# Kernel tuning notes

Measured on AMD Instinct MI355X. Metric: run time of the kernel, lower is better.

## Reference

```python
import jax, jax.numpy as jnp
import numpy as np

N_EXPERTS = 8
TOP_K = 2
D_MODEL = 1024
D_FF = 4 * D_MODEL

def setup_inputs() -> dict:
    key = jax.random.key(0)
    ks = jax.random.split(key, 5)
    s_in = 1.0 / np.sqrt(D_MODEL)
    s_ff = 1.0 / np.sqrt(D_FF)
    return {
        "x": jax.random.normal(ks[0], (2, 2048, D_MODEL), dtype=jnp.float32),
        "Wr": jax.random.normal(ks[1], (N_EXPERTS, D_MODEL), dtype=jnp.float32) * s_in,
        "W1": jax.random.normal(ks[2], (N_EXPERTS, D_FF, D_MODEL), dtype=jnp.float32) * s_in,
        "W2": jax.random.normal(ks[3], (N_EXPERTS, D_MODEL, D_FF), dtype=jnp.float32) * s_ff,
        "W3": jax.random.normal(ks[4], (N_EXPERTS, D_FF, D_MODEL), dtype=jnp.float32) * s_in,
    }

def reference(x, Wr, W1, W2, W3):
    B, S, D = x.shape
    T = B * S
    xf = x.reshape(T, D)
    logits = xf @ Wr.T                         # [T, E]
    probs = jax.nn.softmax(logits, axis=-1)
    top_p, top_i = jax.lax.top_k(probs, TOP_K)  # [T, K]
    top_p = top_p / jnp.sum(top_p, axis=-1, keepdims=True)
    # per-token combine weight for each expert: [T, E]
    onehot = jax.nn.one_hot(top_i, N_EXPERTS, dtype=x.dtype)  # [T, K, E]
    cw = jnp.einsum('tke,tk->te', onehot, top_p)
    out = jnp.zeros_like(xf)
    for e in range(N_EXPERTS):  # fixed small structural loop over experts
        h = jax.nn.silu(xf @ W1[e].T) * (xf @ W3[e].T)  # [T, F]
        y = h @ W2[e].T                                 # [T, D]
        out = out + cw[:, e:e+1] * y
    importance = jnp.sum(probs, axis=0)                 # [E]
    load = jnp.sum(jnp.sum(onehot, axis=1), axis=0)     # [E]
    aux_loss = jnp.sum(importance * load) * (N_EXPERTS / (T ** 2 + 1e-06))
    return out.reshape(B, S, D), aux_loss
```

## Files before the change

kernel.cpp:

```cpp
#include <hip/hip_runtime.h>

#define T_TOK 4096
#define DM 1024
#define DF 4096
#define NE 8
#define BM 256
#define RCAP 10240
#define MAXT 40
#define MAXT2 80
#define ACH_B 32768
#define CHUNK_B 8192

typedef _Float16 f16x8 __attribute__((ext_vector_type(8)));
typedef float f32x4 __attribute__((ext_vector_type(4)));

#define MFMA16(a, b, c) __builtin_amdgcn_mfma_f32_16x16x32_f16(a, b, c, 0, 0, 0)
#define RAW_BAR() __builtin_amdgcn_s_barrier()
#define VMCNT(n) asm volatile("s_waitcnt vmcnt(" #n ")" ::: "memory")

__device__ __forceinline__ ushort f2h_bits(float f) {
    _Float16 h = (_Float16)f;
    return __builtin_bit_cast(unsigned short, h);
}

__device__ __forceinline__ unsigned int pk2(float a, float b) {
    return __builtin_bit_cast(unsigned int, __builtin_amdgcn_cvt_pkrtz(a, b));
}

__device__ __forceinline__ uint4 pack8f(float4 a, float4 b) {
    uint4 r;
    r.x = pk2(a.x, a.y); r.y = pk2(a.z, a.w);
    r.z = pk2(b.x, b.y); r.w = pk2(b.z, b.w);
    return r;
}

__device__ __forceinline__ void gll16(const void* g, void* l) {
    __builtin_amdgcn_global_load_lds(
        (const __attribute__((address_space(1))) unsigned int*)g,
        (__attribute__((address_space(3))) unsigned int*)l, 16, 0, 0);
}

__global__ __launch_bounds__(256) void k_init(float* __restrict__ out,
                                              int* __restrict__ misc,
                                              int* __restrict__ row_tok) {
    int i = blockIdx.x * 256 + threadIdx.x;
    if (i < T_TOK * DM + 1) out[i] = 0.f;
    if (i < RCAP) row_tok[i] = -1;
    if (i < 256) misc[i] = 0;
}

__global__ __launch_bounds__(64) void k_router(const float* __restrict__ x,
                                               const float* __restrict__ Wr,
                                               float* __restrict__ probs,
                                               int* __restrict__ topi,
                                               float* __restrict__ topw,
                                               int* __restrict__ cnt) {
    int t = blockIdx.x;
    int lane = threadIdx.x;
    const float* xr = x + (size_t)t * DM;
    float s[NE];
#pragma unroll
    for (int e = 0; e < NE; e++) s[e] = 0.f;
    for (int j = lane; j < DM; j += 64) {
        float xv = xr[j];
#pragma unroll
        for (int e = 0; e < NE; e++) s[e] += xv * Wr[e * DM + j];
    }
#pragma unroll
    for (int off = 32; off > 0; off >>= 1) {
#pragma unroll
        for (int e = 0; e < NE; e++) s[e] += __shfl_xor(s[e], off, 64);
    }
    if (lane == 0) {
        float mx = s[0];
#pragma unroll
        for (int e = 1; e < NE; e++) mx = fmaxf(mx, s[e]);
        float ex[NE], sum = 0.f;
#pragma unroll
        for (int e = 0; e < NE; e++) { ex[e] = expf(s[e] - mx); sum += ex[e]; }
        float inv = 1.f / sum;
        float p[NE];
#pragma unroll
        for (int e = 0; e < NE; e++) { p[e] = ex[e] * inv; probs[t * NE + e] = p[e]; }
        int i0 = 0;
#pragma unroll
        for (int e = 1; e < NE; e++) if (p[e] > p[i0]) i0 = e;
        int i1 = (i0 == 0) ? 1 : 0;
#pragma unroll
        for (int e = 0; e < NE; e++) if (e != i0 && p[e] > p[i1]) i1 = e;
        float w0 = p[i0], w1 = p[i1], winv = 1.f / (w0 + w1);
        topi[2 * t] = i0;     topw[2 * t] = w0 * winv;
        topi[2 * t + 1] = i1; topw[2 * t + 1] = w1 * winv;
        atomicAdd(&cnt[i0], 1);
        atomicAdd(&cnt[i1], 1);
    }
}

__global__ __launch_bounds__(256) void k_scan(const float* __restrict__ probs,
                                              const int* __restrict__ cnt,
                                              int* __restrict__ poff,
                                              int* __restrict__ texp,
                                              int* __restrict__ texp2,
                                              int* __restrict__ ntp,
                                              float* __restrict__ aux_out) {
    __shared__ float red[256 * NE];
    int tid = threadIdx.x;
    float part[NE];
#pragma unroll
    for (int e = 0; e < NE; e++) part[e] = 0.f;
    for (int t = tid; t < T_TOK; t += 256) {
#pragma unroll
        for (int e = 0; e < NE; e++) part[e] += probs[t * NE + e];
    }
#pragma unroll
    for (int e = 0; e < NE; e++) red[tid * NE + e] = part[e];
    __syncthreads();
    for (int s2 = 128; s2 > 0; s2 >>= 1) {
        if (tid < s2) {
#pragma unroll
            for (int e = 0; e < NE; e++) red[tid * NE + e] += red[(tid + s2) * NE + e];
        }
        __syncthreads();
    }
    if (tid == 0) {
        float al = 0.f;
#pragma unroll
        for (int e = 0; e < NE; e++) al += red[e] * (float)cnt[e];
        *aux_out = al * (8.0f / (16777216.0f + 1e-6f));
        int run = 0, tix = 0;
        for (int e = 0; e < NE; e++) {
            poff[e] = run;
            int nt = (cnt[e] + BM - 1) / BM;
            for (int i = 0; i < nt; i++) texp[tix++] = e;
            run += nt * BM;
        }
        ntp[0] = run / BM;
        ntp[1] = run / 128;
        for (int j = 0; j < MAXT2; j++) texp2[j] = (j >> 1) < tix ? texp[j >> 1] : 0;
    }
}

__global__ __launch_bounds__(256) void k_assign(const int* __restrict__ topi,
                                                const float* __restrict__ topw,
                                                const int* __restrict__ poff,
                                                int* __restrict__ fill,
                                                int* __restrict__ row_tok,
                                                float* __restrict__ row_w) {
    int t = blockIdx.x * 256 + threadIdx.x;
    if (t >= T_TOK) return;
#pragma unroll
    for (int k = 0; k < 2; k++) {
        int e = topi[2 * t + k];
        int pos = atomicAdd(&fill[e], 1);
        int r = poff[e] + pos;
        row_tok[r] = t;
        row_w[r] = topw[2 * t + k];
    }
}

__global__ __launch_bounds__(256) void k_convert(const float* __restrict__ src,
                                                 ushort* __restrict__ dst,
                                                 int row_len) {
    int nk = row_len >> 6;
    int kt = blockIdx.x, rt = blockIdx.y;
    int tid = threadIdx.x;
    int r = tid >> 2, c0 = (tid & 3) * 16;
    const float* s = src + (size_t)(rt * 64 + r) * row_len + kt * 64 + c0;
    float4 v0 = *(const float4*)(s);
    float4 v1 = *(const float4*)(s + 4);
    float4 v2 = *(const float4*)(s + 8);
    float4 v3 = *(const float4*)(s + 12);
    char* chunk = (char*)dst + ((size_t)rt * nk + kt) * CHUNK_B;
    int sw = (r & 7) << 4;
    *(uint4*)(chunk + r * 128 + ((2 * c0) ^ sw)) = pack8f(v0, v1);
    *(uint4*)(chunk + r * 128 + ((2 * c0 + 16) ^ sw)) = pack8f(v2, v3);
}

__global__ __launch_bounds__(512) void k_gather_t(const float* __restrict__ x,
                                                  const int* __restrict__ row_tok,
                                                  ushort* __restrict__ xg) {
    int kt = blockIdx.x, rt = blockIdx.y;
    int tid = threadIdx.x;
    int r = tid >> 1, c0 = (tid & 1) * 32;
    int tok = row_tok[rt * BM + r];
    char* chunk = (char*)xg + ((size_t)rt * 16 + kt) * ACH_B;
    int sw = (r & 7) << 4;
    if (tok >= 0) {
        const float* s = x + (size_t)tok * DM + kt * 64 + c0;
#pragma unroll
        for (int j = 0; j < 4; j++) {
            float4 va = *(const float4*)(s + j * 8);
            float4 vb = *(const float4*)(s + j * 8 + 4);
            *(uint4*)(chunk + r * 128 + ((c0 * 2 + j * 16) ^ sw)) = pack8f(va, vb);
        }
    } else {
        uint4 z = {0, 0, 0, 0};
#pragma unroll
        for (int j = 0; j < 4; j++)
            *(uint4*)(chunk + r * 128 + ((c0 * 2 + j * 16) ^ sw)) = z;
    }
}

__global__ __launch_bounds__(512, 2) void k_g1(const ushort* __restrict__ xg,
                                               const ushort* __restrict__ W1h,
                                               const ushort* __restrict__ W3h,
                                               const int* __restrict__ texp,
                                               const int* __restrict__ ntp,
                                               ushort* __restrict__ hbuf) {
    __shared__ __align__(16) char lds[131072];
    int b = blockIdx.x;
    int sz = (b & 7) * 160 + (b >> 3);
    int ct = sz / MAXT, rt = sz % MAXT;
    if (rt >= ntp[0]) return;
    int e = texp[rt];
    int tid = threadIdx.x, lane = tid & 63, wv = tid >> 6;
    int wr = wv >> 1, wc = wv & 1;

    const char* Ac  = (const char*)xg + (size_t)rt * 16 * ACH_B;
    const char* B1c = (const char*)W1h + ((size_t)(e * 64 + ct * 2) * 16) * CHUNK_B;
    const char* B3c = (const char*)W3h + ((size_t)(e * 64 + ct * 2) * 16) * CHUNK_B;

    const f32x4 fz = {0.f, 0.f, 0.f, 0.f};
    f32x4 acc1[4][4], acc3[4][4];
#pragma unroll
    for (int m = 0; m < 4; m++)
#pragma unroll
        for (int n = 0; n < 4; n++) { acc1[m][n] = fz; acc3[m][n] = fz; }

    f16x8 af[4], bf[4];
    int kb_base = (lane >> 4) * 16;

#define ST_A(kt_, b_, h_) {                                                        \
        const char* s_ = Ac + (kt_) * ACH_B + (h_) * 16384 + wv * 2048 + lane * 16; \
        char* d_ = lds + (b_) * 65536 + (h_) * 16384 + wv * 2048;                   \
        gll16(s_, d_); gll16(s_ + 1024, d_ + 1024); }
#define ST_B(Bc_, kt_, b_, off_) {                                                          \
        gll16(Bc_ + (kt_) * 8192 + wv * 1024 + lane * 16,                                    \
              lds + (b_) * 65536 + (off_) + wv * 1024);                                      \
        gll16(Bc_ + 131072 + (kt_) * 8192 + wv * 1024 + lane * 16,                           \
              lds + (b_) * 65536 + (off_) + 8192 + wv * 1024); }
#define DS_A(b_, ks_) _Pragma("unroll") for (int m = 0; m < 4; m++) {              \
        int r_ = wr * 64 + m * 16 + (lane & 15);                                   \
        af[m] = *(const f16x8*)(lds + (b_) * 65536 + r_ * 128 +                    \
                                 (((ks_) * 64 + kb_base) ^ ((r_ & 7) << 4))); }
#define DS_B(b_, off_, ks_) _Pragma("unroll") for (int n = 0; n < 4; n++) {        \
        int c_ = wc * 64 + n * 16 + (lane & 15);                                   \
        bf[n] = *(const f16x8*)(lds + (b_) * 65536 + (off_) + c_ * 128 +           \
                                 (((ks_) * 64 + kb_base) ^ ((c_ & 7) << 4))); }
#define MM(accX) _Pragma("unroll") for (int n = 0; n < 4; n++)                     \
        _Pragma("unroll") for (int m = 0; m < 4; m++)                              \
            accX[m][n] = MFMA16(af[m], bf[n], accX[m][n]);

    ST_A(0, 0, 0); ST_A(0, 0, 1); ST_B(B1c, 0, 0, 32768); ST_B(B3c, 0, 0, 49152);
    VMCNT(2);
    RAW_BAR();

    for (int it = 0; it < 8; ++it) {
        int t1 = 2 * it + 1;
        int t2 = 2 * it + 2;
        DS_A(0, 0); DS_B(0, 32768, 0);
        ST_A(t1, 1, 0);
        RAW_BAR();
        __builtin_amdgcn_s_setprio(1); MM(acc1); __builtin_amdgcn_s_setprio(0);
        VMCNT(2);
        RAW_BAR();
        DS_B(0, 49152, 0);
        ST_A(t1, 1, 1);
        RAW_BAR();
        __builtin_amdgcn_s_setprio(1); MM(acc3); __builtin_amdgcn_s_setprio(0);
        RAW_BAR();
        DS_A(0, 1); DS_B(0, 32768, 1);
        ST_B(B1c, t1, 1, 32768);
        RAW_BAR();
        __builtin_amdgcn_s_setprio(1); MM(acc1); __builtin_amdgcn_s_setprio(0);
        RAW_BAR();
        DS_B(0, 49152, 1);
        ST_B(B3c, t1, 1, 49152);
        RAW_BAR();
        __builtin_amdgcn_s_setprio(1); MM(acc3); __builtin_amdgcn_s_setprio(0);
        VMCNT(2);
        RAW_BAR();
        DS_A(1, 0); DS_B(1, 32768, 0);
        if (it < 7) ST_A(t2, 0, 0);
        RAW_BAR();
        __builtin_amdgcn_s_setprio(1); MM(acc1); __builtin_amdgcn_s_setprio(0);
        if (it < 7) { VMCNT(2); } else { VMCNT(0); }
        RAW_BAR();
        DS_B(1, 49152, 0);
        if (it < 7) ST_A(t2, 0, 1);
        RAW_BAR();
        __builtin_amdgcn_s_setprio(1); MM(acc3); __builtin_amdgcn_s_setprio(0);
        RAW_BAR();
        DS_A(1, 1); DS_B(1, 32768, 1);
        if (it < 7) ST_B(B1c, t2, 0, 32768);
        RAW_BAR();
        __builtin_amdgcn_s_setprio(1); MM(acc1); __builtin_amdgcn_s_setprio(0);
        RAW_BAR();
        DS_B(1, 49152, 1);
        if (it < 7) ST_B(B3c, t2, 0, 49152);
        RAW_BAR();
        __builtin_amdgcn_s_setprio(1); MM(acc3); __builtin_amdgcn_s_setprio(0);
        if (it < 7) { VMCNT(2); }
        RAW_BAR();
    }
#undef ST_A
#undef ST_B
#undef DS_A
#undef DS_B
#undef MM

#pragma unroll
    for (int m = 0; m < 4; m++) {
#pragma unroll
        for (int i = 0; i < 4; i++) {
            int rl = wr * 64 + m * 16 + (lane >> 4) * 4 + i;
            int sw = (rl & 7) << 4;
#pragma unroll
            for (int n = 0; n < 4; n++) {
                int fl = wc * 64 + n * 16 + (lane & 15);
                float a1 = acc1[m][n][i], a3 = acc3[m][n][i];
                float h = (a1 / (1.f + expf(-a1))) * a3;
                char* hc = (char*)hbuf + ((size_t)rt * 64 + ct * 2 + (fl >> 6)) * ACH_B;
                *(ushort*)(hc + rl * 128 + ((2 * (fl & 63)) ^ sw)) = f2h_bits(h);
            }
        }
    }
}

__global__ __launch_bounds__(256, 2) void k_g2(const ushort* __restrict__ hbuf,
                                               const ushort* __restrict__ W2h,
                                               const int* __restrict__ texp2,
                                               const int* __restrict__ ntp,
                                               const int* __restrict__ row_tok,
                                               const float* __restrict__ row_w,
                                               float* __restrict__ out) {
    __shared__ __align__(16) char lds[73728];
    int b = blockIdx.x;
    int sz = (b & 7) * 160 + (b >> 3);
    int ct = sz / MAXT2, rt2 = sz % MAXT2;
    if (rt2 >= ntp[1]) return;
    int e = texp2[rt2];
    int tid = threadIdx.x, lane = tid & 63, wv = tid >> 6;
    int wr = wv >> 1, wc = wv & 1;

    const char* Ac = (const char*)hbuf + ((size_t)(rt2 >> 1) * 64) * ACH_B + (rt2 & 1) * 16384;
    const char* Bc = (const char*)W2h + ((size_t)(e * 16 + ct) * 64) * CHUNK_B;

    const f32x4 fz = {0.f, 0.f, 0.f, 0.f};
    f32x4 acc[4][2];
#pragma unroll
    for (int m = 0; m < 4; m++)
#pragma unroll
        for (int n = 0; n < 2; n++) acc[m][n] = fz;

    f16x8 af[4], bf[2];
    int kb_base = (lane >> 4) * 16;

#define BUF3(t_) (((t_) % 3) * 24576)
#define ST2_A(kt_) {                                                                 \
        const char* s_ = Ac + (size_t)(kt_) * ACH_B + wv * 4096 + lane * 16;         \
        char* d_ = lds + BUF3(kt_) + wv * 4096;                                      \
        gll16(s_, d_); gll16(s_ + 1024, d_ + 1024);                                  \
        gll16(s_ + 2048, d_ + 2048); gll16(s_ + 3072, d_ + 3072); }
#define ST2_B(kt_) {                                                                 \
        const char* s_ = Bc + (size_t)(kt_) * 8192 + wv * 2048 + lane * 16;          \
        char* d_ = lds + BUF3(kt_) + 16384 + wv * 2048;                              \
        gll16(s_, d_); gll16(s_ + 1024, d_ + 1024); }
#define DS2_A(bo_, ks_) _Pragma("unroll") for (int m = 0; m < 4; m++) {              \
        int r_ = wr * 64 + m * 16 + (lane & 15);                                     \
        af[m] = *(const f16x8*)(lds + (bo_) + r_ * 128 +                             \
                                 (((ks_) * 64 + kb_base) ^ ((r_ & 7) << 4))); }
#define DS2_B(bo_, ks_) _Pragma("unroll") for (int n = 0; n < 2; n++) {              \
        int c_ = wc * 32 + n * 16 + (lane & 15);                                     \
        bf[n] = *(const f16x8*)(lds + (bo_) + 16384 + c_ * 128 +                     \
                                 (((ks_) * 64 + kb_base) ^ ((c_ & 7) << 4))); }
#define MM2() _Pragma("unroll") for (int n = 0; n < 2; n++)                          \
        _Pragma("unroll") for (int m = 0; m < 4; m++)                                \
            acc[m][n] = MFMA16(af[m], bf[n], acc[m][n]);

    ST2_A(0); ST2_B(0);
    ST2_A(1); ST2_B(1);
    VMCNT(6);
    RAW_BAR();

    for (int t = 0; t < 64; ++t) {
        int bo = BUF3(t);
        DS2_A(bo, 0); DS2_B(bo, 0);
        if (t < 62) ST2_A(t + 2);
        RAW_BAR();
        __builtin_amdgcn_s_setprio(1); MM2(); __builtin_amdgcn_s_setprio(0);
        RAW_BAR();
        DS2_A(bo, 1); DS2_B(bo, 1);
        if (t < 62) ST2_B(t + 2);
        RAW_BAR();
        __builtin_amdgcn_s_setprio(1); MM2(); __builtin_amdgcn_s_setprio(0);
        if (t < 62) { VMCNT(6); }
        else if (t == 62) { VMCNT(0); }
        RAW_BAR();
    }
#undef BUF3
#undef ST2_A
#undef ST2_B
#undef DS2_A
#undef DS2_B
#undef MM2

#pragma unroll
    for (int m = 0; m < 4; m++) {
#pragma unroll
        for (int i = 0; i < 4; i++) {
            int rr = rt2 * 128 + wr * 64 + m * 16 + (lane >> 4) * 4 + i;
            int tok = row_tok[rr];
            if (tok >= 0) {
                float w = row_w[rr];
                float* orow = out + (size_t)tok * DM + ct * 64 + wc * 32 + (lane & 15);
#pragma unroll
                for (int n = 0; n < 2; n++) atomicAdd(&orow[n * 16], w * acc[m][n][i]);
            }
        }
    }
}

extern "C" void kernel_launch(void* const* d_in, const int* in_sizes, int n_in,
                              void* d_out, int out_size, void* d_ws, size_t ws_size,
                              hipStream_t stream) {
    (void)in_sizes; (void)n_in; (void)out_size; (void)ws_size;
    const float* x  = (const float*)d_in[0];
    const float* Wr = (const float*)d_in[1];
    const float* W1 = (const float*)d_in[2];
    const float* W2 = (const float*)d_in[3];
    const float* W3 = (const float*)d_in[4];
    float* out = (float*)d_out;
    char* ws = (char*)d_ws;

    int* misc  = (int*)ws;
    int* cnt   = misc;
    int* fill  = misc + 8;
    int* poff  = misc + 16;
    int* texp  = misc + 24;
    int* texp2 = misc + 64;
    int* ntp   = misc + 144;
    int*    topi    = (int*)(ws + 1024);
    float*  topw    = (float*)(ws + 33792);
    float*  probs   = (float*)(ws + 66560);
    int*    row_tok = (int*)(ws + 197632);
    float*  row_w   = (float*)(ws + 238592);
    ushort* hbuf    = (ushort*)(ws + 279552);
    ushort* W1h     = (ushort*)(ws + 84165632);
    ushort* W3h     = (ushort*)(ws + 151274496);
    ushort* xg      = (ushort*)(ws + 218383360);
    ushort* W2h     = (ushort*)(ws + 218383360);

    k_init<<<(T_TOK * DM + 1 + 255) / 256, 256, 0, stream>>>(out, misc, row_tok);
    k_router<<<T_TOK, 64, 0, stream>>>(x, Wr, probs, topi, topw, cnt);
    k_scan<<<1, 256, 0, stream>>>(probs, cnt, poff, texp, texp2, ntp, out + (size_t)T_TOK * DM);
    k_assign<<<(T_TOK + 255) / 256, 256, 0, stream>>>(topi, topw, poff, fill, row_tok, row_w);

    k_convert<<<dim3(16, 512), 256, 0, stream>>>(W1, W1h, DM);
    k_convert<<<dim3(16, 512), 256, 0, stream>>>(W3, W3h, DM);
    k_gather_t<<<dim3(16, MAXT), 512, 0, stream>>>(x, row_tok, xg);
    k_g1<<<32 * MAXT, 512, 0, stream>>>(xg, W1h, W3h, texp, ntp, hbuf);
    k_convert<<<dim3(64, 128), 256, 0, stream>>>(W2, W2h, DF);
    k_g2<<<8 * MAXT2 * 2, 256, 0, stream>>>(hbuf, W2h, texp2, ntp, row_tok, row_w, out);
}
```

Before: 677.9 us.

## Map GEMM blocks to XCDs by expert via precomputed block tables

The scan kernel now builds block-to-tile tables for both grouped GEMMs. Each table routes all tiles of one expert to the same blockIdx residue mod 8, and so to the same XCD, spilling to the next XCD once 160 slots fill. The aim is to keep each expert's weights in a single XCD's L2 and so cut duplicate weight fetches. The cost is a serial single-thread loop in k_scan and an extra indirect load per block, and load across XCDs may be uneven when experts get unequal token counts.

Measured after the change: 820.4 us. 1.21x slower.

```diff
diff --git a/kernel.cpp b/kernel.cpp
--- a/kernel.cpp
+++ b/kernel.cpp
@@ -101,7 +101,8 @@
                                               int* __restrict__ poff,
                                               int* __restrict__ texp,
                                               int* __restrict__ texp2,
-                                              int* __restrict__ ntp,
+                                              int* __restrict__ bmap1,
+                                              int* __restrict__ bmap2,
                                               float* __restrict__ aux_out) {
     __shared__ float red[256 * NE];
     int tid = threadIdx.x;
@@ -122,21 +123,46 @@
         }
         __syncthreads();
     }
+    for (int s = tid; s < 1280; s += 256) { bmap1[s] = -1; bmap2[s] = -1; }
+    __syncthreads();
     if (tid == 0) {
         float al = 0.f;
 #pragma unroll
         for (int e = 0; e < NE; e++) al += red[e] * (float)cnt[e];
         *aux_out = al * (8.0f / (16777216.0f + 1e-6f));
         int run = 0, tix = 0;
+        int tstart[NE], ntv[NE];
         for (int e = 0; e < NE; e++) {
             poff[e] = run;
             int nt = (cnt[e] + BM - 1) / BM;
+            tstart[e] = tix; ntv[e] = nt;
             for (int i = 0; i < nt; i++) texp[tix++] = e;
             run += nt * BM;
         }
-        ntp[0] = run / BM;
-        ntp[1] = run / 128;
         for (int j = 0; j < MAXT2; j++) texp2[j] = (j >> 1) < tix ? texp[j >> 1] : 0;
+        int u1[NE] = {0, 0, 0, 0, 0, 0, 0, 0};
+        for (int e = 0; e < NE; e++)
+            for (int i = 0; i < ntv[e]; i++) {
+                int rt = tstart[e] + i;
+                for (int ct = 0; ct < 32; ct++) {
+                    int k = e, tr = 0;
+                    while (u1[k] >= 160 && tr < 8) { k = (k + 1) & 7; tr++; }
+                    bmap1[k + 8 * u1[k]] = (rt << 5) | ct;
+                    u1[k]++;
+                }
+            }
+        int u2[NE] = {0, 0, 0, 0, 0, 0, 0, 0};
+        for (int e = 0; e < NE; e++)
+            for (int i = 0; i < ntv[e]; i++)
+                for (int h = 0; h < 2; h++) {
+                    int rt2 = (tstart[e] + i) * 2 + h;
+                    for (int ct = 0; ct < 16; ct++) {
+                        int k = e, tr = 0;
+                        while (u2[k] >= 160 && tr < 8) { k = (k + 1) & 7; tr++; }
+                        bmap2[k + 8 * u2[k]] = (rt2 << 4) | ct;
+                        u2[k]++;
+                    }
+                }
     }
 }
 
@@ -205,13 +231,12 @@
                                                const ushort* __restrict__ W1h,
                                                const ushort* __restrict__ W3h,
                                                const int* __restrict__ texp,
-                                               const int* __restrict__ ntp,
+                                               const int* __restrict__ bmap1,
                                                ushort* __restrict__ hbuf) {
     __shared__ __align__(16) char lds[131072];
-    int b = blockIdx.x;
-    int sz = (b & 7) * 160 + (b >> 3);
-    int ct = sz / MAXT, rt = sz % MAXT;
-    if (rt >= ntp[0]) return;
+    int mcode = bmap1[blockIdx.x];
+    if (mcode < 0) return;
+    int rt = mcode >> 5, ct = mcode & 31;
     int e = texp[rt];
     int tid = threadIdx.x, lane = tid & 63, wv = tid >> 6;
     int wr = wv >> 1, wc = wv & 1;
@@ -330,15 +355,14 @@
 __global__ __launch_bounds__(256, 2) void k_g2(const ushort* __restrict__ hbuf,
                                                const ushort* __restrict__ W2h,
                                                const int* __restrict__ texp2,
-                                               const int* __restrict__ ntp,
+                                               const int* __restrict__ bmap2,
                                                const int* __restrict__ row_tok,
                                                const float* __restrict__ row_w,
                                                float* __restrict__ out) {
     __shared__ __align__(16) char lds[73728];
-    int b = blockIdx.x;
-    int sz = (b & 7) * 160 + (b >> 3);
-    int ct = sz / MAXT2, rt2 = sz % MAXT2;
-    if (rt2 >= ntp[1]) return;
+    int mcode = bmap2[blockIdx.x];
+    if (mcode < 0) return;
+    int rt2 = mcode >> 4, ct = mcode & 15;
     int e = texp2[rt2];
     int tid = threadIdx.x, lane = tid & 63, wv = tid >> 6;
     int wr = wv >> 1, wc = wv & 1;
@@ -439,27 +463,29 @@
     int* poff  = misc + 16;
     int* texp  = misc + 24;
     int* texp2 = misc + 64;
-    int* ntp   = misc + 144;
     int*    topi    = (int*)(ws + 1024);
     float*  topw    = (float*)(ws + 33792);
     float*  probs   = (float*)(ws + 66560);
     int*    row_tok = (int*)(ws + 197632);
     float*  row_w   = (float*)(ws + 238592);
-    ushort* hbuf    = (ushort*)(ws + 279552);
-    ushort* W1h     = (ushort*)(ws + 84165632);
-    ushort* W3h     = (ushort*)(ws + 151274496);
-    ushort* xg      = (ushort*)(ws + 218383360);
-    ushort* W2h     = (ushort*)(ws + 218383360);
+    int*    bmap1   = (int*)(ws + 279552);
+    int*    bmap2   = (int*)(ws + 284672);
+    ushort* hbuf    = (ushort*)(ws + 294912);
+    ushort* W1h     = (ushort*)(ws + 84180992);
+    ushort* W3h     = (ushort*)(ws + 151289856);
+    ushort* xg      = (ushort*)(ws + 218398720);
+    ushort* W2h     = (ushort*)(ws + 218398720);
 
     k_init<<<(T_TOK * DM + 1 + 255) / 256, 256, 0, stream>>>(out, misc, row_tok);
     k_router<<<T_TOK, 64, 0, stream>>>(x, Wr, probs, topi, topw, cnt);
-    k_scan<<<1, 256, 0, stream>>>(probs, cnt, poff, texp, texp2, ntp, out + (size_t)T_TOK * DM);
+    k_scan<<<1, 256, 0, stream>>>(probs, cnt, poff, texp, texp2, bmap1, bmap2,
+                                  out + (size_t)T_TOK * DM);
     k_assign<<<(T_TOK + 255) / 256, 256, 0, stream>>>(topi, topw, poff, fill, row_tok, row_w);
 
     k_convert<<<dim3(16, 512), 256, 0, stream>>>(W1, W1h, DM);
     k_convert<<<dim3(16, 512), 256, 0, stream>>>(W3, W3h, DM);
     k_gather_t<<<dim3(16, MAXT), 512, 0, stream>>>(x, row_tok, xg);
-    k_g1<<<32 * MAXT, 512, 0, stream>>>(xg, W1h, W3h, texp, ntp, hbuf);
+    k_g1<<<1280, 512, 0, stream>>>(xg, W1h, W3h, texp, bmap1, hbuf);
     k_convert<<<dim3(64, 128), 256, 0, stream>>>(W2, W2h, DF);
-    k_g2<<<8 * MAXT2 * 2, 256, 0, stream>>>(hbuf, W2h, texp2, ntp, row_tok, row_w, out);
-}
+    k_g2<<<1280, 256, 0, stream>>>(hbuf, W2h, texp2, bmap2, row_tok, row_w, out);
+}
```
